# Kernel tuning notes

Measured on AMD Instinct MI355X. Metric: run time of the kernel, lower is better.

The kernel has to match this reference:

```python
import jax, jax.numpy as jnp
import numpy as np

EPS = 1e-6                                   # VN leaky-relu denominator eps
BN_SCALE = np.float32(1.0 / np.sqrt(1.0 + 1e-5))  # eval-mode BatchNorm with default stats
NEG = 0.2                                    # negative_slope


def vn_lin(x, w):
    # x: [n, c, 3, ...]; w: [c, o] -> [n, o, 3, ...]
    return jnp.einsum('nc...,co->no...', x, w)


def vn_act(p, d):
    # Vector-Neuron leaky ReLU: project p off the half-space defined by direction d.
    dot = jnp.sum(p * d, axis=2, keepdims=True)
    dsq = jnp.sum(d * d, axis=2, keepdims=True)
    corr = p - (dot / (dsq + EPS)) * d
    return NEG * p + (1.0 - NEG) * jnp.where(dot >= 0, p, corr)


def score_net(x, w_vn, wd_vn, w_h1, w_h2, b_h2, temp=1.0):
    # CorrelationNet: VNLinearLeakyReLU(3 -> 2*ks) -> norm -> 1x1 convs -> softmax
    p = vn_lin(x, w_vn) * BN_SCALE           # [N, 2ks, 3, K] (VNBatchNorm ~ scalar in eval)
    d = vn_lin(x, wd_vn)
    s = vn_act(p, d)
    s = jnp.linalg.norm(s, axis=2)           # [N, 2ks, K]
    s = jax.nn.relu(jnp.einsum('nck,co->nok', s, w_h1) * BN_SCALE)  # conv1d k=1, BN, relu
    s = jnp.einsum('nck,co->nok', s, w_h2) + b_h2[None, :, None]     # last conv with bias
    return jax.nn.softmax(s / temp, axis=1)  # [N, ks, K]


def setup_inputs() -> dict:
    key = jax.random.key(0)
    k = [jax.random.fold_in(key, i) for i in range(13)]
    N, N2, K, KS, OUT = 16000, 20000, 16, 8, 64
    half = OUT // 2
    return {
        'q_pts': jax.random.normal(k[0], (N, 3), jnp.float32),
        's_pts': jax.random.normal(k[1], (N2, 3), jnp.float32),
        's_feats': jax.random.normal(k[2], (N2, 1, 3), jnp.float32),
        'neighbor_indices': jax.random.randint(k[3], (N, K), 0, N2),
        'wb': jax.random.normal(k[4], (3, KS * half), jnp.float32) * np.float32(np.sqrt(2.0 / 3.0)),
        'w_vn': jax.random.normal(k[5], (3, 2 * KS), jnp.float32) * 0.5,
        'wd_vn': jax.random.normal(k[6], (3, 2 * KS), jnp.float32) * 0.5,
        'w_h1': jax.random.normal(k[7], (2 * KS, KS), jnp.float32) * 0.25,
        'w_h2': jax.random.normal(k[8], (KS, KS), jnp.float32) * 0.35,
        'b_h2': jnp.zeros((KS,), jnp.float32),
        'wd_relu': jax.random.normal(k[9], (half, half), jnp.float32) * 0.18,
        'w_un': jax.random.normal(k[10], (half, OUT), jnp.float32) * 0.18,
        'wd_un': jax.random.normal(k[11], (half, OUT), jnp.float32) * 0.18,
    }


def reference(q_pts, s_pts, s_feats, neighbor_indices, wb, w_vn, wd_vn,
              w_h1, w_h2, b_h2, wd_relu, w_un, wd_un):
    N, K = neighbor_indices.shape
    KS = w_h2.shape[1]
    # neighbor gather + centering: [N, K, 3] -> [N, 1, 3, K]
    pts = s_pts[neighbor_indices] - q_pts[:, None]
    pts = jnp.transpose(pts, (0, 2, 1))[:, None]
    centers = jnp.broadcast_to(jnp.mean(pts, axis=-1, keepdims=True), pts.shape)
    cross = jnp.cross(pts, centers, axis=2)
    local = jnp.concatenate([pts, centers, cross], axis=1)   # [N, 3, 3, K]
    scores = score_net(local, w_vn, wd_vn, w_h1, w_h2, b_h2)  # [N, KS, K]
    # kernel-point correlation conv
    pro = jnp.einsum('ncdk,cf->nfdk', local, wb)              # [N, KS*half, 3, K]
    pro = pro.reshape(N, KS, -1, 3, K)
    pro = jnp.sum(pro * scores[:, :, None, None, :], axis=1)  # [N, half, 3, K]
    nrm = jnp.linalg.norm(pro, axis=2, keepdims=True)
    normed = pro / jnp.maximum(nrm, 1e-12)                    # F.normalize(p=2, dim=2)
    feats = jnp.mean(normed, axis=-1)                         # [N, half, 3]
    feats = vn_act(feats, vn_lin(feats, wd_relu))             # VNLeakyReLU
    out = vn_act(vn_lin(feats, w_un) * BN_SCALE, vn_lin(feats, wd_un))  # VNLinearLeakyReLU
    return out                                                # [N, out_dim, 3]
```

## Files before the change

### kernel.cpp

```cpp
#include <hip/hip_runtime.h>
#include <math.h>

#define VN_EPS   1e-6f
#define NEG      0.2f
#define POS      0.8f

template <int CTRL>
__device__ __forceinline__ float dpp_add(float v) {
    int s = __builtin_amdgcn_update_dpp(0, __float_as_int(v), CTRL, 0xf, 0xf, true);
    return v + __int_as_float(s);
}

__device__ __forceinline__ float row16_allsum(float v) {
    v = dpp_add<0x128>(v);
    v = dpp_add<0x124>(v);
    v = dpp_add<0x122>(v);
    v = dpp_add<0x121>(v);
    return v;
}

__device__ __forceinline__ float row16_sum15(float v) {
    v = dpp_add<0x118>(v);
    v = dpp_add<0x114>(v);
    v = dpp_add<0x112>(v);
    v = dpp_add<0x111>(v);
    return v;
}

__global__ __launch_bounds__(256) void areconv_kernel(
    const float* __restrict__ q_pts,
    const float* __restrict__ s_pts,
    const int*   __restrict__ nbr,
    const float* __restrict__ wb,
    const float* __restrict__ w_vn,
    const float* __restrict__ wd_vn,
    const float* __restrict__ w_h1,
    const float* __restrict__ w_h2,
    const float* __restrict__ b_h2,
    const float* __restrict__ wd_relu,
    const float* __restrict__ w_un,
    const float* __restrict__ wd_un,
    float* __restrict__ out,
    int N)
{
    const float BN_SCALE = 0.999994993f;

    __shared__ float feats [4][104];
    __shared__ float feats2[4][104];

    const int tid  = threadIdx.x;
    const int wv   = tid >> 6;
    const int lane = tid & 63;
    const int g    = (tid >> 4) & 3;
    const int k    = tid & 15;
    const int n    = blockIdx.x * 4 + wv;
    if (n >= N) return;

    const float qx = q_pts[n * 3 + 0];
    const float qy = q_pts[n * 3 + 1];
    const float qz = q_pts[n * 3 + 2];
    const int   id = nbr[n * 16 + k];
    const float px = s_pts[id * 3 + 0] - qx;
    const float py = s_pts[id * 3 + 1] - qy;
    const float pz = s_pts[id * 3 + 2] - qz;

    const float cx = row16_allsum(px) * 0.0625f;
    const float cy = row16_allsum(py) * 0.0625f;
    const float cz = row16_allsum(pz) * 0.0625f;

    const float rx = py * cz - pz * cy;
    const float ry = pz * cx - px * cz;
    const float rz = px * cy - py * cx;

    const float L[3][3] = {{px, py, pz}, {cx, cy, cz}, {rx, ry, rz}};

    float sn_loc[4];
#pragma unroll
    for (int j = 0; j < 4; ++j) {
        const int o = g * 4 + j;
        const float wv0 = w_vn[o],  wv1 = w_vn[16 + o],  wv2 = w_vn[32 + o];
        const float wd0 = wd_vn[o], wd1 = wd_vn[16 + o], wd2 = wd_vn[32 + o];
        float pv[3], dv[3];
        float dot = 0.f, dsq = 0.f;
#pragma unroll
        for (int d = 0; d < 3; ++d) {
            const float pp = BN_SCALE * (L[0][d] * wv0 + L[1][d] * wv1 + L[2][d] * wv2);
            const float dd = L[0][d] * wd0 + L[1][d] * wd1 + L[2][d] * wd2;
            pv[d] = pp; dv[d] = dd;
            dot += pp * dd;
            dsq += dd * dd;
        }
        const float f = dot * __builtin_amdgcn_rcpf(dsq + VN_EPS);
        float acc = 0.f;
#pragma unroll
        for (int d = 0; d < 3; ++d) {
            const float corr = pv[d] - f * dv[d];
            const float sel  = (dot >= 0.f) ? pv[d] : corr;
            const float a    = NEG * pv[d] + POS * sel;
            acc += a * a;
        }
        sn_loc[j] = __builtin_amdgcn_sqrtf(acc);
    }

    float tt[8];
#pragma unroll
    for (int o = 0; o < 8; ++o) {
        float t = sn_loc[0] * w_h1[(g * 4 + 0) * 8 + o]
                + sn_loc[1] * w_h1[(g * 4 + 1) * 8 + o]
                + sn_loc[2] * w_h1[(g * 4 + 2) * 8 + o]
                + sn_loc[3] * w_h1[(g * 4 + 3) * 8 + o];
        t += __shfl_xor(t, 16);
        t += __shfl_xor(t, 32);
        tt[o] = fmaxf(t * BN_SCALE, 0.f);
    }

    float sc[8];
    float mx = -1e30f;
#pragma unroll
    for (int o = 0; o < 8; ++o) {
        float u = b_h2[o];
#pragma unroll
        for (int c = 0; c < 8; ++c) u += tt[c] * w_h2[c * 8 + o];
        sc[o] = u;
        mx = fmaxf(mx, u);
    }
    float se = 0.f;
#pragma unroll
    for (int o = 0; o < 8; ++o) { sc[o] = __expf(sc[o] - mx); se += sc[o]; }
    const float inv_se = __builtin_amdgcn_rcpf(se);
#pragma unroll
    for (int o = 0; o < 8; ++o) sc[o] *= inv_se;

#pragma unroll
    for (int i = 0; i < 8; ++i) {
        const int h = g * 8 + i;
        float w0 = 0.f, w1 = 0.f, w2 = 0.f;
#pragma unroll
        for (int s = 0; s < 8; ++s) {
            const float sv = sc[s];
            w0 += sv * wb[0 * 256 + s * 32 + h];
            w1 += sv * wb[1 * 256 + s * 32 + h];
            w2 += sv * wb[2 * 256 + s * 32 + h];
        }
        const float v0 = L[0][0] * w0 + L[1][0] * w1 + L[2][0] * w2;
        const float v1 = L[0][1] * w0 + L[1][1] * w1 + L[2][1] * w2;
        const float v2 = L[0][2] * w0 + L[1][2] * w1 + L[2][2] * w2;
        const float vv   = v0 * v0 + v1 * v1 + v2 * v2;
        const float innr = __builtin_amdgcn_rsqf(fmaxf(vv, 1e-24f));
        const float x0 = row16_sum15(v0 * innr);
        const float x1 = row16_sum15(v1 * innr);
        const float x2 = row16_sum15(v2 * innr);
        if (k == 15) {
            feats[wv][h * 3 + 0] = x0 * 0.0625f;
            feats[wv][h * 3 + 1] = x1 * 0.0625f;
            feats[wv][h * 3 + 2] = x2 * 0.0625f;
        }
    }

    {
        const int o    = lane >> 1;
        const int half = lane & 1;
        float d0 = 0.f, d1 = 0.f, d2 = 0.f;
#pragma unroll 8
        for (int i = 0; i < 16; ++i) {
            const int h = half * 16 + i;
            const float w = wd_relu[h * 32 + o];
            d0 += feats[wv][h * 3 + 0] * w;
            d1 += feats[wv][h * 3 + 1] * w;
            d2 += feats[wv][h * 3 + 2] * w;
        }
        d0 += __shfl_xor(d0, 1);
        d1 += __shfl_xor(d1, 1);
        d2 += __shfl_xor(d2, 1);
        const float p0 = feats[wv][o * 3 + 0];
        const float p1 = feats[wv][o * 3 + 1];
        const float p2 = feats[wv][o * 3 + 2];
        const float dot = p0 * d0 + p1 * d1 + p2 * d2;
        const float dsq = d0 * d0 + d1 * d1 + d2 * d2;
        const float f   = dot * __builtin_amdgcn_rcpf(dsq + VN_EPS);
        const bool  pos = (dot >= 0.f);
        if (half == 0) {
            feats2[wv][o * 3 + 0] = NEG * p0 + POS * (pos ? p0 : (p0 - f * d0));
            feats2[wv][o * 3 + 1] = NEG * p1 + POS * (pos ? p1 : (p1 - f * d1));
            feats2[wv][o * 3 + 2] = NEG * p2 + POS * (pos ? p2 : (p2 - f * d2));
        }
    }

    {
        const int o = lane;
        float u0 = 0.f, u1 = 0.f, u2 = 0.f;
        float v0 = 0.f, v1 = 0.f, v2 = 0.f;
#pragma unroll 8
        for (int h = 0; h < 32; ++h) {
            const float a0 = feats2[wv][h * 3 + 0];
            const float a1 = feats2[wv][h * 3 + 1];
            const float a2 = feats2[wv][h * 3 + 2];
            const float wu = w_un[h * 64 + o];
            const float wd = wd_un[h * 64 + o];
            u0 += a0 * wu; u1 += a1 * wu; u2 += a2 * wu;
            v0 += a0 * wd; v1 += a1 * wd; v2 += a2 * wd;
        }
        u0 *= BN_SCALE; u1 *= BN_SCALE; u2 *= BN_SCALE;
        const float dot = u0 * v0 + u1 * v1 + u2 * v2;
        const float dsq = v0 * v0 + v1 * v1 + v2 * v2;
        const float f   = dot * __builtin_amdgcn_rcpf(dsq + VN_EPS);
        const bool  pos = (dot >= 0.f);
        const long  base = (long)n * 192 + o * 3;
        out[base + 0] = NEG * u0 + POS * (pos ? u0 : (u0 - f * v0));
        out[base + 1] = NEG * u1 + POS * (pos ? u1 : (u1 - f * v1));
        out[base + 2] = NEG * u2 + POS * (pos ? u2 : (u2 - f * v2));
    }
}

extern "C" void kernel_launch(void* const* d_in, const int* in_sizes, int n_in,
                              void* d_out, int out_size, void* d_ws, size_t ws_size,
                              hipStream_t stream) {
    const float* q_pts   = (const float*)d_in[0];
    const float* s_pts   = (const float*)d_in[1];
    const int*   nbr     = (const int*)  d_in[3];
    const float* wb      = (const float*)d_in[4];
    const float* w_vn    = (const float*)d_in[5];
    const float* wd_vn   = (const float*)d_in[6];
    const float* w_h1    = (const float*)d_in[7];
    const float* w_h2    = (const float*)d_in[8];
    const float* b_h2    = (const float*)d_in[9];
    const float* wd_relu = (const float*)d_in[10];
    const float* w_un    = (const float*)d_in[11];
    const float* wd_un   = (const float*)d_in[12];
    float* out = (float*)d_out;

    const int N = in_sizes[0] / 3;
    const int blocks = (N + 3) / 4;
    areconv_kernel<<<blocks, 256, 0, stream>>>(
        q_pts, s_pts, nbr, wb, w_vn, wd_vn, w_h1, w_h2, b_h2,
        wd_relu, w_un, wd_un, out, N);
}
```

Baseline: 128.6 us.

## Vectorize weight loads and transpose shared feats to component-major layout

Switches the small-matrix stages to 2- and 4-wide vector types so weight loads and FMAs can use wider global/LDS accesses and packed math. The shared feature buffers move from interleaved [h*3+d] to component-major [d][h], which allows float4 LDS reads and writes. It also adds a min-blocks hint to launch_bounds to push occupancy. In exchange, register pressure may rise, and the per-lane gathers of wd_relu and w_un stay scalar.

```diff
diff --git a/kernel.cpp b/kernel.cpp
--- a/kernel.cpp
+++ b/kernel.cpp
@@ -4,13 +4,15 @@
 #define VN_EPS   1e-6f
 #define NEG      0.2f
 #define POS      0.8f
+
+typedef float v2f __attribute__((ext_vector_type(2)));
+typedef float v4f __attribute__((ext_vector_type(4)));
 
 template <int CTRL>
 __device__ __forceinline__ float dpp_add(float v) {
     int s = __builtin_amdgcn_update_dpp(0, __float_as_int(v), CTRL, 0xf, 0xf, true);
     return v + __int_as_float(s);
 }
-
 __device__ __forceinline__ float row16_allsum(float v) {
     v = dpp_add<0x128>(v);
     v = dpp_add<0x124>(v);
@@ -18,7 +20,6 @@
     v = dpp_add<0x121>(v);
     return v;
 }
-
 __device__ __forceinline__ float row16_sum15(float v) {
     v = dpp_add<0x118>(v);
     v = dpp_add<0x114>(v);
@@ -27,7 +28,7 @@
     return v;
 }
 
-__global__ __launch_bounds__(256) void areconv_kernel(
+__global__ __launch_bounds__(256, 4) void areconv_kernel(
     const float* __restrict__ q_pts,
     const float* __restrict__ s_pts,
     const int*   __restrict__ nbr,
@@ -45,8 +46,8 @@
 {
     const float BN_SCALE = 0.999994993f;
 
-    __shared__ float feats [4][104];
-    __shared__ float feats2[4][104];
+    __shared__ float featsA [4][3][36];
+    __shared__ float feats2A[4][3][36];
 
     const int tid  = threadIdx.x;
     const int wv   = tid >> 6;
@@ -104,25 +105,29 @@
 
     float tt[8];
 #pragma unroll
-    for (int o = 0; o < 8; ++o) {
-        float t = sn_loc[0] * w_h1[(g * 4 + 0) * 8 + o]
-                + sn_loc[1] * w_h1[(g * 4 + 1) * 8 + o]
-                + sn_loc[2] * w_h1[(g * 4 + 2) * 8 + o]
-                + sn_loc[3] * w_h1[(g * 4 + 3) * 8 + o];
-        t += __shfl_xor(t, 16);
-        t += __shfl_xor(t, 32);
-        tt[o] = fmaxf(t * BN_SCALE, 0.f);
+    for (int op = 0; op < 4; ++op) {
+        v2f t = sn_loc[0] * (*(const v2f*)&w_h1[(g * 4 + 0) * 8 + 2 * op])
+              + sn_loc[1] * (*(const v2f*)&w_h1[(g * 4 + 1) * 8 + 2 * op])
+              + sn_loc[2] * (*(const v2f*)&w_h1[(g * 4 + 2) * 8 + 2 * op])
+              + sn_loc[3] * (*(const v2f*)&w_h1[(g * 4 + 3) * 8 + 2 * op]);
+        float t0 = t[0], t1 = t[1];
+        t0 += __shfl_xor(t0, 16);  t0 += __shfl_xor(t0, 32);
+        t1 += __shfl_xor(t1, 16);  t1 += __shfl_xor(t1, 32);
+        tt[2 * op + 0] = fmaxf(t0 * BN_SCALE, 0.f);
+        tt[2 * op + 1] = fmaxf(t1 * BN_SCALE, 0.f);
     }
 
     float sc[8];
     float mx = -1e30f;
 #pragma unroll
-    for (int o = 0; o < 8; ++o) {
-        float u = b_h2[o];
-#pragma unroll
-        for (int c = 0; c < 8; ++c) u += tt[c] * w_h2[c * 8 + o];
-        sc[o] = u;
-        mx = fmaxf(mx, u);
+    for (int op = 0; op < 4; ++op) {
+        v2f u = *(const v2f*)&b_h2[2 * op];
+#pragma unroll
+        for (int c = 0; c < 8; ++c)
+            u += tt[c] * (*(const v2f*)&w_h2[c * 8 + 2 * op]);
+        sc[2 * op + 0] = u[0];
+        sc[2 * op + 1] = u[1];
+        mx = fmaxf(mx, fmaxf(u[0], u[1]));
     }
     float se = 0.f;
 #pragma unroll
@@ -132,75 +137,97 @@
     for (int o = 0; o < 8; ++o) sc[o] *= inv_se;
 
 #pragma unroll
-    for (int i = 0; i < 8; ++i) {
-        const int h = g * 8 + i;
-        float w0 = 0.f, w1 = 0.f, w2 = 0.f;
-#pragma unroll
-        for (int s = 0; s < 8; ++s) {
+    for (int pg = 0; pg < 2; ++pg) {
+        const int hb = g * 8 + pg * 4;
+        v4f W0 = sc[0] * (*(const v4f*)&wb[0 * 256 + hb]);
+        v4f W1 = sc[0] * (*(const v4f*)&wb[1 * 256 + hb]);
+        v4f W2 = sc[0] * (*(const v4f*)&wb[2 * 256 + hb]);
+#pragma unroll
+        for (int s = 1; s < 8; ++s) {
             const float sv = sc[s];
-            w0 += sv * wb[0 * 256 + s * 32 + h];
-            w1 += sv * wb[1 * 256 + s * 32 + h];
-            w2 += sv * wb[2 * 256 + s * 32 + h];
-        }
-        const float v0 = L[0][0] * w0 + L[1][0] * w1 + L[2][0] * w2;
-        const float v1 = L[0][1] * w0 + L[1][1] * w1 + L[2][1] * w2;
-        const float v2 = L[0][2] * w0 + L[1][2] * w1 + L[2][2] * w2;
-        const float vv   = v0 * v0 + v1 * v1 + v2 * v2;
-        const float innr = __builtin_amdgcn_rsqf(fmaxf(vv, 1e-24f));
-        const float x0 = row16_sum15(v0 * innr);
-        const float x1 = row16_sum15(v1 * innr);
-        const float x2 = row16_sum15(v2 * innr);
+            W0 += sv * (*(const v4f*)&wb[0 * 256 + s * 32 + hb]);
+            W1 += sv * (*(const v4f*)&wb[1 * 256 + s * 32 + hb]);
+            W2 += sv * (*(const v4f*)&wb[2 * 256 + s * 32 + hb]);
+        }
+        v4f V0 = L[0][0] * W0 + L[1][0] * W1 + L[2][0] * W2;
+        v4f V1 = L[0][1] * W0 + L[1][1] * W1 + L[2][1] * W2;
+        v4f V2 = L[0][2] * W0 + L[1][2] * W1 + L[2][2] * W2;
+        v4f vv = V0 * V0 + V1 * V1 + V2 * V2;
+        v4f inn;
+#pragma unroll
+        for (int e = 0; e < 4; ++e)
+            inn[e] = __builtin_amdgcn_rsqf(fmaxf(vv[e], 1e-24f)) * 0.0625f;
+        V0 *= inn; V1 *= inn; V2 *= inn;
+        v4f X0, X1, X2;
+#pragma unroll
+        for (int e = 0; e < 4; ++e) {
+            X0[e] = row16_sum15(V0[e]);
+            X1[e] = row16_sum15(V1[e]);
+            X2[e] = row16_sum15(V2[e]);
+        }
         if (k == 15) {
-            feats[wv][h * 3 + 0] = x0 * 0.0625f;
-            feats[wv][h * 3 + 1] = x1 * 0.0625f;
-            feats[wv][h * 3 + 2] = x2 * 0.0625f;
+            *(v4f*)&featsA[wv][0][hb] = X0;
+            *(v4f*)&featsA[wv][1][hb] = X1;
+            *(v4f*)&featsA[wv][2][hb] = X2;
         }
     }
 
     {
         const int o    = lane >> 1;
         const int half = lane & 1;
-        float d0 = 0.f, d1 = 0.f, d2 = 0.f;
-#pragma unroll 8
-        for (int i = 0; i < 16; ++i) {
-            const int h = half * 16 + i;
-            const float w = wd_relu[h * 32 + o];
-            d0 += feats[wv][h * 3 + 0] * w;
-            d1 += feats[wv][h * 3 + 1] * w;
-            d2 += feats[wv][h * 3 + 2] * w;
-        }
+        v4f a0 = {0.f, 0.f, 0.f, 0.f}, a1 = a0, a2 = a0;
+#pragma unroll
+        for (int grp = 0; grp < 4; ++grp) {
+            const int hb = half * 16 + grp * 4;
+            const v4f w4 = { wd_relu[(hb + 0) * 32 + o], wd_relu[(hb + 1) * 32 + o],
+                             wd_relu[(hb + 2) * 32 + o], wd_relu[(hb + 3) * 32 + o] };
+            a0 += (*(const v4f*)&featsA[wv][0][hb]) * w4;
+            a1 += (*(const v4f*)&featsA[wv][1][hb]) * w4;
+            a2 += (*(const v4f*)&featsA[wv][2][hb]) * w4;
+        }
+        float d0 = a0[0] + a0[1] + a0[2] + a0[3];
+        float d1 = a1[0] + a1[1] + a1[2] + a1[3];
+        float d2 = a2[0] + a2[1] + a2[2] + a2[3];
         d0 += __shfl_xor(d0, 1);
         d1 += __shfl_xor(d1, 1);
         d2 += __shfl_xor(d2, 1);
-        const float p0 = feats[wv][o * 3 + 0];
-        const float p1 = feats[wv][o * 3 + 1];
-        const float p2 = feats[wv][o * 3 + 2];
+        const float p0 = featsA[wv][0][o];
+        const float p1 = featsA[wv][1][o];
+        const float p2 = featsA[wv][2][o];
         const float dot = p0 * d0 + p1 * d1 + p2 * d2;
         const float dsq = d0 * d0 + d1 * d1 + d2 * d2;
         const float f   = dot * __builtin_amdgcn_rcpf(dsq + VN_EPS);
         const bool  pos = (dot >= 0.f);
         if (half == 0) {
-            feats2[wv][o * 3 + 0] = NEG * p0 + POS * (pos ? p0 : (p0 - f * d0));
-            feats2[wv][o * 3 + 1] = NEG * p1 + POS * (pos ? p1 : (p1 - f * d1));
-            feats2[wv][o * 3 + 2] = NEG * p2 + POS * (pos ? p2 : (p2 - f * d2));
+            feats2A[wv][0][o] = NEG * p0 + POS * (pos ? p0 : (p0 - f * d0));
+            feats2A[wv][1][o] = NEG * p1 + POS * (pos ? p1 : (p1 - f * d1));
+            feats2A[wv][2][o] = NEG * p2 + POS * (pos ? p2 : (p2 - f * d2));
         }
     }
 
     {
         const int o = lane;
-        float u0 = 0.f, u1 = 0.f, u2 = 0.f;
-        float v0 = 0.f, v1 = 0.f, v2 = 0.f;
-#pragma unroll 8
-        for (int h = 0; h < 32; ++h) {
-            const float a0 = feats2[wv][h * 3 + 0];
-            const float a1 = feats2[wv][h * 3 + 1];
-            const float a2 = feats2[wv][h * 3 + 2];
-            const float wu = w_un[h * 64 + o];
-            const float wd = wd_un[h * 64 + o];
-            u0 += a0 * wu; u1 += a1 * wu; u2 += a2 * wu;
-            v0 += a0 * wd; v1 += a1 * wd; v2 += a2 * wd;
-        }
-        u0 *= BN_SCALE; u1 *= BN_SCALE; u2 *= BN_SCALE;
+        v4f au0 = {0.f, 0.f, 0.f, 0.f}, au1 = au0, au2 = au0;
+        v4f av0 = au0, av1 = au0, av2 = au0;
+#pragma unroll
+        for (int grp = 0; grp < 8; ++grp) {
+            const int hb = grp * 4;
+            const v4f f0 = *(const v4f*)&feats2A[wv][0][hb];
+            const v4f f1 = *(const v4f*)&feats2A[wv][1][hb];
+            const v4f f2 = *(const v4f*)&feats2A[wv][2][hb];
+            const v4f wu = { w_un[(hb + 0) * 64 + o], w_un[(hb + 1) * 64 + o],
+                             w_un[(hb + 2) * 64 + o], w_un[(hb + 3) * 64 + o] };
+            const v4f wd = { wd_un[(hb + 0) * 64 + o], wd_un[(hb + 1) * 64 + o],
+                             wd_un[(hb + 2) * 64 + o], wd_un[(hb + 3) * 64 + o] };
+            au0 += f0 * wu; au1 += f1 * wu; au2 += f2 * wu;
+            av0 += f0 * wd; av1 += f1 * wd; av2 += f2 * wd;
+        }
+        float u0 = (au0[0] + au0[1] + au0[2] + au0[3]) * BN_SCALE;
+        float u1 = (au1[0] + au1[1] + au1[2] + au1[3]) * BN_SCALE;
+        float u2 = (au2[0] + au2[1] + au2[2] + au2[3]) * BN_SCALE;
+        float v0 = av0[0] + av0[1] + av0[2] + av0[3];
+        float v1 = av1[0] + av1[1] + av1[2] + av1[3];
+        float v2 = av2[0] + av2[1] + av2[2] + av2[3];
         const float dot = u0 * v0 + u1 * v1 + u2 * v2;
         const float dsq = v0 * v0 + v1 * v1 + v2 * v2;
         const float f   = dot * __builtin_amdgcn_rcpf(dsq + VN_EPS);
```

Measured after the change: 127.2 us. Within noise of the previous version (-1.0%).
